# Performance work log

Hardware: AMD Instinct MI355X
Metric: run time of the kernel (lower is better)

Reference implementation:

```python
import jax, jax.numpy as jnp
import numpy as np

N, D_MODEL, NUM_HEAD = 2, 256, 8
HI, WI = 40, 40
MAX_DIS = 7
WS = 2 * MAX_DIS + 1          # 15
HD = D_MODEL // NUM_HEAD      # 32
T = HD ** 0.5
NEG = 1e8                     # fp32 mask value used by the torch module


def setup_inputs() -> dict:
    key = jax.random.key(0)
    ks = jax.random.split(key, 10)
    s = 0.02
    f = lambda i, shape: jax.random.normal(ks[i], shape, jnp.float32)
    return dict(
        q=f(0, (N, D_MODEL, HI, WI)),
        k=f(1, (N, D_MODEL, HI, WI)),
        v=f(2, (N, D_MODEL, HI, WI)),
        Wq=f(3, (D_MODEL, D_MODEL)) * s, bq=jnp.zeros((D_MODEL,), jnp.float32),
        Wk=f(4, (D_MODEL, D_MODEL)) * s, bk=jnp.zeros((D_MODEL,), jnp.float32),
        Wv=f(5, (D_MODEL, D_MODEL)) * s, bv=jnp.zeros((D_MODEL,), jnp.float32),
        rel_k_w=f(6, (NUM_HEAD, WS * WS, HD)) * s,      # grouped 1x1 conv weight
        rel_k_b=jnp.zeros((NUM_HEAD, WS * WS), jnp.float32),
        rel_v=f(7, (NUM_HEAD, HD, WS * WS)) * s,        # nn.Parameter (zeros in torch; random here to exercise math)
        Wp=f(8, (D_MODEL, D_MODEL)) * s, bp=jnp.zeros((D_MODEL,), jnp.float32),
    )


def _geometry(h, w):
    # Static (numpy) index/mask construction matching compute_mask().
    qy = np.repeat(np.arange(h), w)
    qx = np.tile(np.arange(w), h)
    dy = qy[None, :] - qy[:, None]          # key - query, [hw, hw]
    dx = qx[None, :] - qx[:, None]
    valid = (np.abs(dy) <= MAX_DIS) & (np.abs(dx) <= MAX_DIS)
    widx = (np.clip(dy + MAX_DIS, 0, WS - 1) * WS + np.clip(dx + MAX_DIS, 0, WS - 1))
    offs = np.arange(-MAX_DIS, MAX_DIS + 1)
    dyo = np.repeat(offs, WS)               # [ws*ws] row-major window order (dy*WS+dx)
    dxo = np.tile(offs, WS)
    ky = qy[:, None] + dyo[None, :]         # [hw, ws*ws]
    kx = qx[:, None] + dxo[None, :]
    in_img = (ky >= 0) & (ky < h) & (kx >= 0) & (kx < w)
    jidx = np.clip(ky, 0, h - 1) * w + np.clip(kx, 0, w - 1)
    return (jnp.asarray(valid), jnp.asarray(widx), jnp.asarray(in_img), jnp.asarray(jidx))


def reference(q, k, v, Wq, bq, Wk, bk, Wv, bv, rel_k_w, rel_k_b, rel_v, Wp, bp):
    n, c, h, w = q.shape
    hw = h * w
    nh, hd = NUM_HEAD, c // NUM_HEAD

    def proj(x, Wt, b):  # 1x1 conv == per-pixel linear
        return jnp.einsum('oc,ncp->nop', Wt, x.reshape(n, c, hw)) + b[None, :, None]

    qf = proj(q, Wq, bq)
    kf = proj(k, Wk, bk)
    vf = proj(v, Wv, bv)

    qh = qf.reshape(n, nh, hd, hw)
    kh = kf.reshape(n, nh, hd, hw)
    vh = vf.reshape(n, nh, hd, hw)

    # grouped 1x1 conv: per-head linear from hd channels to ws*ws (computed BEFORE q/T)
    rel = jnp.einsum('hwd,nhdp->nhpw', rel_k_w, qh) + rel_k_b[None, :, None, :]  # [n,nh,hw,ws2]

    qh = qh / T
    qk = jnp.einsum('nhdi,nhdj->nhij', qh, kh)   # [n,nh,hw,hw]

    valid, widx, in_img, jidx = _geometry(h, w)

    # --- 'global' path: dense hw x hw, non-local keys masked with -1e8, local keys get rel bias ---
    rel_dense = jnp.take_along_axis(rel, widx[None, None], axis=3)   # [n,nh,hw,hw]
    global_logits = jnp.where(valid[None, None], qk + rel_dense, qk - NEG)
    global_attn = jax.nn.softmax(global_logits, axis=-1)
    agg_value = jnp.einsum('nhij,nhdj->inhd', global_attn, vh).reshape(hw, n, c)

    # --- local path: gather ws*ws window per query; out-of-image keys are -1e8 (pad value), rel added everywhere ---
    gathered = jnp.take_along_axis(qk, jidx[None, None], axis=3)     # [n,nh,hw,ws2]
    local_logits = jnp.where(in_img[None, None], gathered, -NEG) + rel
    local_attn = jax.nn.softmax(local_logits, axis=-1)
    agg_bias = jnp.einsum('nhiw,hdw->inhd', local_attn, rel_v).reshape(hw, n, c)

    out = (agg_value + agg_bias) @ Wp.T + bp    # nn.Linear, output [hw, n, c]
    return out, local_attn
```

## Files before the change

kernel.cpp:

```cpp
#include <hip/hip_runtime.h>
#include <hip/hip_bf16.h>

#define HW    1600
#define NB    2
#define NHEAD 8
#define HD    32
#define WS2   225
#define WDIM  40
#define CDIM  256
#define PROJ  819200
#define RELSTR 248
#define TSC   5.656854249492381f

typedef __attribute__((ext_vector_type(8))) short short8;
typedef __attribute__((ext_vector_type(4))) short short4v;
typedef __attribute__((ext_vector_type(4))) float floatx4;

static __device__ __forceinline__ float bu2f(short u) {
    return __uint_as_float(((unsigned)(unsigned short)u) << 16);
}
static __device__ __forceinline__ short f2bu(float f) {
    __hip_bfloat16 h = __float2bfloat16(f);
    short s; __builtin_memcpy(&s, &h, 2); return s;
}
static __device__ __forceinline__ unsigned pk2(short a, short b) {
    return (unsigned)(unsigned short)a | ((unsigned)(unsigned short)b << 16);
}
static __device__ __forceinline__ float ldf(const void* p, size_t i, bool f32) {
    return f32 ? ((const float*)p)[i] : __bfloat162float(((const __hip_bfloat16*)p)[i]);
}
static __device__ __forceinline__ void st_out(void* p, size_t i, float v, bool f32) {
    if (f32) ((float*)p)[i] = v;
    else     ((__hip_bfloat16*)p)[i] = __float2bfloat16(v);
}

__global__ __launch_bounds__(256) void prep_kernel(
    const void* __restrict__ q, const void* __restrict__ relv,
    const void* __restrict__ Wq, const void* __restrict__ Wk,
    const void* __restrict__ Wv, const void* __restrict__ Wp,
    const void* __restrict__ bq, const void* __restrict__ bk,
    const void* __restrict__ bv, const void* __restrict__ bp,
    const void* __restrict__ rkw, const void* __restrict__ rkb,
    int* __restrict__ flag, __hip_bfloat16* __restrict__ relvT,
    __hip_bfloat16* __restrict__ Wqb, __hip_bfloat16* __restrict__ Wkb,
    __hip_bfloat16* __restrict__ Wvb, __hip_bfloat16* __restrict__ Wpb,
    float* __restrict__ bqf, float* __restrict__ bkf,
    float* __restrict__ bvf, float* __restrict__ bpf,
    __hip_bfloat16* __restrict__ rkwb, __hip_bfloat16* __restrict__ rkbb)
{
    __shared__ int sbad;
    if (threadIdx.x == 0) sbad = 0;
    __syncthreads();
    int bad = 0;
    const __hip_bfloat16* qb = (const __hip_bfloat16*)q;
    for (int i = threadIdx.x; i < 4096; i += 256) {
        float v = __bfloat162float(qb[i]);
        if (!(v > -1e6f && v < 1e6f)) bad = 1;
    }
    if (bad) sbad = 1;
    __syncthreads();
    const bool f32 = (sbad != 0);
    if (blockIdx.x == 0 && threadIdx.x == 0) *flag = sbad;

    const int gid = blockIdx.x * 256 + threadIdx.x;
    const int gsz = gridDim.x * 256;

    for (int e = gid; e < NHEAD * WS2 * HD; e += gsz) {
        const int h = e / (WS2 * HD), idx = e - h * (WS2 * HD);
        const int w = idx >> 5, d = idx & 31;
        relvT[e] = __float2bfloat16(ldf(relv, ((size_t)h * HD + d) * WS2 + w, f32));
    }
    for (int e = gid; e < CDIM * CDIM; e += gsz) {
        Wqb[e] = __float2bfloat16(ldf(Wq, e, f32));
        Wkb[e] = __float2bfloat16(ldf(Wk, e, f32));
        Wvb[e] = __float2bfloat16(ldf(Wv, e, f32));
        Wpb[e] = __float2bfloat16(ldf(Wp, e, f32));
    }
    for (int e = gid; e < CDIM; e += gsz) {
        bqf[e] = ldf(bq, e, f32); bkf[e] = ldf(bk, e, f32);
        bvf[e] = ldf(bv, e, f32); bpf[e] = ldf(bp, e, f32);
    }
    for (int e = gid; e < NHEAD * WS2 * HD; e += gsz)
        rkwb[e] = __float2bfloat16(ldf(rkw, e, f32));
    for (int e = gid; e < NHEAD * WS2; e += gsz)
        rkbb[e] = __float2bfloat16(ldf(rkb, e, f32));
}

__global__ __launch_bounds__(512) void proj_fused(
    const void* __restrict__ xq, const void* __restrict__ xk, const void* __restrict__ xv,
    const __hip_bfloat16* __restrict__ Wqb, const float* __restrict__ bqf,
    const __hip_bfloat16* __restrict__ Wkb, const float* __restrict__ bkf,
    const __hip_bfloat16* __restrict__ Wvb, const float* __restrict__ bvf,
    const int* __restrict__ flag,
    __hip_bfloat16* __restrict__ qs, __hip_bfloat16* __restrict__ ks,
    __hip_bfloat16* __restrict__ vs)
{
    __shared__ short xt[32][264];
    const bool f32 = (*flag != 0);
    const int tid = threadIdx.x;
    const int m0 = blockIdx.x * 32;
    const int n  = blockIdx.y;
    const int t  = blockIdx.z;
    const void* x; const short* W; const float* bias; __hip_bfloat16* dst; float scale;
    if (t == 0)      { x = xq; W = (const short*)Wqb; bias = bqf; dst = qs; scale = 0.17677669529663687f; }
    else if (t == 1) { x = xk; W = (const short*)Wkb; bias = bkf; dst = ks; scale = 1.f; }
    else             { x = xv; W = (const short*)Wvb; bias = bvf; dst = vs; scale = 1.f; }

    {
        const int c  = tid & 255;
        const int gh = tid >> 8;
        const size_t xb = ((size_t)n * CDIM + c) * HW + m0 + gh * 16;
        if (f32) {
            const float* xr = (const float*)x + xb;
            #pragma unroll
            for (int g = 0; g < 4; ++g) {
                float4 f = *(const float4*)(xr + g * 4);
                xt[gh*16 + g*4+0][c] = f2bu(f.x); xt[gh*16 + g*4+1][c] = f2bu(f.y);
                xt[gh*16 + g*4+2][c] = f2bu(f.z); xt[gh*16 + g*4+3][c] = f2bu(f.w);
            }
        } else {
            const __hip_bfloat16* xr = (const __hip_bfloat16*)x + xb;
            short8 s0 = *(const short8*)(xr);
            short8 s1 = *(const short8*)(xr + 8);
            #pragma unroll
            for (int u = 0; u < 8; ++u) {
                xt[gh*16 + u][c]     = s0[u];
                xt[gh*16 + 8 + u][c] = s1[u];
            }
        }
    }
    __syncthreads();

    const int wave = tid >> 6, lane = tid & 63;
    const int m = lane & 15, qd = lane >> 4;

    short8 A[2][8];
    #pragma unroll
    for (int mt = 0; mt < 2; ++mt)
        #pragma unroll
        for (int k = 0; k < 8; ++k)
            A[mt][k] = *(const short8*)(&xt[mt*16 + m][k*32 + qd*8]);

    #pragma unroll
    for (int og = 0; og < 2; ++og) {
        const int o0 = (wave * 2 + og) * 16;
        short8 B[8];
        #pragma unroll
        for (int k = 0; k < 8; ++k)
            B[k] = *(const short8*)(W + (size_t)(o0 + m) * CDIM + k*32 + qd*8);
        floatx4 acc0 = {0,0,0,0}, acc1 = {0,0,0,0};
        #pragma unroll
        for (int k = 0; k < 8; ++k) {
            acc0 = __builtin_amdgcn_mfma_f32_16x16x32_bf16(A[0][k], B[k], acc0, 0, 0, 0);
            acc1 = __builtin_amdgcn_mfma_f32_16x16x32_bf16(A[1][k], B[k], acc1, 0, 0, 0);
        }
        const int o = o0 + (lane & 15), h = o >> 5, d = o & 31;
        const float bv_ = bias[o];
        #pragma unroll
        for (int rg = 0; rg < 4; ++rg) {
            const int p = m0 + (lane >> 4) * 4 + rg;
            dst[((size_t)(n*NHEAD + h)*HW + p)*HD + d]      = __float2bfloat16((acc0[rg] + bv_) * scale);
            dst[((size_t)(n*NHEAD + h)*HW + p + 16)*HD + d] = __float2bfloat16((acc1[rg] + bv_) * scale);
        }
    }
}

#define SP_OFF    0
#define R2_OFF    15616
#define R1_OFF    24064
#define SMAX_OFF  39680
#define SSUM_OFF  39936
#define SMEM_SZ   40192

__global__ __launch_bounds__(256) void attn_mfma(
    const __hip_bfloat16* __restrict__ qs, const __hip_bfloat16* __restrict__ ks,
    const __hip_bfloat16* __restrict__ vs,
    const short* __restrict__ rkwb, const short* __restrict__ rkbb,
    const __hip_bfloat16* __restrict__ relvT,
    const int* __restrict__ flag,
    __hip_bfloat16* __restrict__ agg,
    void* __restrict__ dout)
{
    __shared__ __align__(16) char smem[SMEM_SZ];
    short* sP   = (short*)(smem + SP_OFF);
    short* sRel = (short*)(smem + R2_OFF);
    short* sPw  = (short*)(smem + R2_OFF);
    short* sB   = (short*)(smem + R1_OFF);
    float* sOh  = (float*)(smem + R1_OFF);
    float* sMax = (float*)(smem + SMAX_OFF);
    float* sSum = (float*)(smem + SSUM_OFF);

    const bool f32 = (*flag != 0);
    const int tid = threadIdx.x;
    const int wave = tid >> 6, lane = tid & 63;
    const int m = lane & 15, quad = lane >> 4;
    const int y = blockIdx.x / 3, tile3 = blockIdx.x % 3;
    const int x0 = (tile3 == 0) ? 0 : (tile3 == 1) ? 16 : 24;
    const int wlo = (tile3 == 2) ? 8 : 0;
    const int nh_ = blockIdx.y;
    const int h = nh_ & 7, n = nh_ >> 3;
    const size_t qb = (size_t)nh_ * HW;
    const size_t qrow0 = qb + (size_t)y * WDIM + x0;

    const short8 afrag = *(const short8*)((const short*)qs + (qrow0 + m) * HD + quad * 8);

    for (int wt = wave; wt < 15; wt += 4) {
        const int w0 = wt * 16;
        const int wl = min(w0 + m, WS2 - 1);
        const short8 B = *(const short8*)(rkwb + ((size_t)h * WS2 + wl) * HD + quad * 8);
        floatx4 acc = {0.f, 0.f, 0.f, 0.f};
        acc = __builtin_amdgcn_mfma_f32_16x16x32_bf16(afrag, B, acc, 0, 0, 0);
        const int wcol = w0 + m;
        if (wcol < WS2) {
            const float rb_ = bu2f(rkbb[(size_t)h * WS2 + wcol]);
            #pragma unroll
            for (int rg = 0; rg < 4; ++rg)
                sRel[(quad * 4 + rg) * RELSTR + wcol] = f2bu(acc[rg] * TSC + rb_);
        }
    }
    __syncthreads();

    float L[8][4];
    #pragma unroll
    for (int j = 0; j < 8; ++j)
        #pragma unroll
        for (int rg = 0; rg < 4; ++rg) L[j][rg] = -1e30f;

    #pragma unroll
    for (int j = 0; j < 8; ++j) {
        const int t = wave + 4 * j;
        if (t < 30) {
            const int r = t >> 1, c0_ = (t & 1) << 4;
            const int cc = c0_ + m;
            const int ky = y + r - 7, kxl = x0 - 7 + cc;
            const int gky = min(max(ky, 0), WDIM - 1), gkx = min(max(kxl, 0), WDIM - 1);
            const short8 kfrag = *(const short8*)((const short*)ks + (qb + (size_t)gky * WDIM + gkx) * HD + quad * 8);
            floatx4 s4 = {0.f, 0.f, 0.f, 0.f};
            s4 = __builtin_amdgcn_mfma_f32_16x16x32_bf16(kfrag, afrag, s4, 0, 0, 0);
            const bool kyok = (unsigned)ky < (unsigned)WDIM;
            #pragma unroll
            for (int rg = 0; rg < 4; ++rg) {
                const int kkc = c0_ + quad * 4 + rg;
                const int kx = x0 - 7 + kkc;
                const int dx7 = kkc - m;
                if (kyok && (unsigned)kx < (unsigned)WDIM && (unsigned)dx7 < 15u)
                    L[j][rg] = s4[rg] + bu2f(sRel[m * RELSTR + r * 15 + dx7]);
            }
        }
    }

    float mx = L[0][0];
    #pragma unroll
    for (int j = 0; j < 8; ++j)
        #pragma unroll
        for (int rg = 0; rg < 4; ++rg) mx = fmaxf(mx, L[j][rg]);
    mx = fmaxf(mx, __shfl_xor(mx, 16));
    mx = fmaxf(mx, __shfl_xor(mx, 32));
    if (lane < 16) sMax[lane * 4 + wave] = mx;
    __syncthreads();
    const float4 vM = *(const float4*)&sMax[m * 4];
    const float M = fmaxf(fmaxf(vM.x, vM.y), fmaxf(vM.z, vM.w));
    float sm = 0.f;
    #pragma unroll
    for (int j = 0; j < 8; ++j)
        #pragma unroll
        for (int rg = 0; rg < 4; ++rg) { L[j][rg] = __expf(L[j][rg] - M); sm += L[j][rg]; }
    sm += __shfl_xor(sm, 16);
    sm += __shfl_xor(sm, 32);
    if (lane < 16) sSum[lane * 4 + wave] = sm;
    __syncthreads();
    const float4 vS = *(const float4*)&sSum[m * 4];
    const float inv = 1.f / (vS.x + vS.y + vS.z + vS.w);

    for (int e = tid; e < 16 * 39; e += 256) {
        const int row = e / 39, idx = e - row * 39;
        const int c = (idx < 15) ? idx * 16 + 15 : 240 + (idx - 15);
        sPw[row * 264 + c] = 0;
    }

    #pragma unroll
    for (int j = 0; j < 8; ++j) {
        const int t = wave + 4 * j;
        if (t < 30) {
            const int r = t >> 1, c0_ = (t & 1) << 4;
            const int kb = c0_ + quad * 4;
            short4v pk;
            #pragma unroll
            for (int rg = 0; rg < 4; ++rg) pk[rg] = f2bu(L[j][rg] * inv);
            *(short4v*)(sP + m * 488 + r * 32 + kb) = pk;
            #pragma unroll
            for (int rg = 0; rg < 4; ++rg) {
                const int dx7 = kb + rg - m;
                if ((unsigned)dx7 < 15u) sPw[m * 264 + r * 16 + dx7] = pk[rg];
            }
        }
    }
    __syncthreads();

    #pragma unroll
    for (int rr = 0; rr < 4; ++rr) {
        const int qm = wave * 4 + rr;
        if (qm >= wlo) {
            const size_t obase = (size_t)PROJ + (qrow0 + qm) * WS2;
            #pragma unroll
            for (int c = 0; c < 4; ++c) {
                const int col = lane + 64 * c;
                if (col < WS2) {
                    const int rq = col / 15, dxq = col - rq * 15;
                    st_out(dout, obase + col, bu2f(sPw[qm * 264 + rq * 16 + dxq]), f32);
                }
            }
        }
    }

    for (int half = 0; half < 2; ++half) {
        __syncthreads();
        const int h16 = half << 4;
        {
            unsigned* dstw = (unsigned*)sB;
            for (int p = tid; p < 240; p += 256) {
                const int kk0 = 2 * p;
                const int r = kk0 >> 5, c = kk0 & 31;
                const int gky = min(max(y + r - 7, 0), WDIM - 1);
                const int gkx0 = min(max(x0 - 7 + c, 0), WDIM - 1);
                const int gkx1 = min(max(x0 - 7 + c + 1, 0), WDIM - 1);
                const short* v0 = (const short*)vs + (qb + (size_t)gky * WDIM + gkx0) * HD + h16;
                const short* v1 = (const short*)vs + (qb + (size_t)gky * WDIM + gkx1) * HD + h16;
                const short8 a0 = *(const short8*)v0, b0 = *(const short8*)v1;
                const short8 a1 = *(const short8*)(v0 + 8), b1 = *(const short8*)(v1 + 8);
                #pragma unroll
                for (int dd = 0; dd < 8; ++dd) dstw[dd * 244 + p] = pk2(a0[dd], b0[dd]);
                #pragma unroll
                for (int dd = 0; dd < 8; ++dd) dstw[(dd + 8) * 244 + p] = pk2(a1[dd], b1[dd]);
            }
        }
        __syncthreads();
        floatx4 acc = {0.f, 0.f, 0.f, 0.f};
        for (int u = wave; u < 15; u += 4) {
            const short8 Af = *(const short8*)(sP + m * 488 + u * 32 + quad * 8);
            const short8 Bf = *(const short8*)(sB + m * 488 + u * 32 + quad * 8);
            acc = __builtin_amdgcn_mfma_f32_16x16x32_bf16(Af, Bf, acc, 0, 0, 0);
        }
        __syncthreads();
        {
            unsigned* dstw = (unsigned*)sB;
            for (int p = tid; p < 132; p += 256) {
                short8 a0 = {0,0,0,0,0,0,0,0}, a1 = a0, b0 = a0, b1 = a0;
                if (p < 120) {
                    const int kcol0 = 2 * p;
                    const int r = kcol0 >> 4, dx = kcol0 & 15;
                    const int w0 = r * 15 + dx;
                    const short* rp = (const short*)relvT + ((size_t)h * WS2 + w0) * HD + h16;
                    a0 = *(const short8*)rp; a1 = *(const short8*)(rp + 8);
                    if (dx < 14) {
                        const short* rq = (const short*)relvT + ((size_t)h * WS2 + w0 + 1) * HD + h16;
                        b0 = *(const short8*)rq; b1 = *(const short8*)(rq + 8);
                    }
                }
                #pragma unroll
                for (int dd = 0; dd < 8; ++dd) dstw[dd * 132 + p] = pk2(a0[dd], b0[dd]);
                #pragma unroll
                for (int dd = 0; dd < 8; ++dd) dstw[(dd + 8) * 132 + p] = pk2(a1[dd], b1[dd]);
            }
        }
        __syncthreads();
        for (int u = wave; u < 8; u += 4) {
            const short8 Af = *(const short8*)(sPw + m * 264 + u * 32 + quad * 8);
            const short8 Bf = *(const short8*)(sB + m * 264 + u * 32 + quad * 8);
            acc = __builtin_amdgcn_mfma_f32_16x16x32_bf16(Af, Bf, acc, 0, 0, 0);
        }
        __syncthreads();
        #pragma unroll
        for (int rg = 0; rg < 4; ++rg)
            sOh[wave * 256 + (quad * 4 + rg) * 16 + m] = acc[rg];
        __syncthreads();
        {
            const int qq = tid >> 4, dd = tid & 15;
            const float s = sOh[tid] + sOh[256 + tid] + sOh[512 + tid] + sOh[768 + tid];
            if (qq >= wlo) {
                const size_t i = (size_t)y * WDIM + x0 + qq;
                agg[(i * NB + n) * CDIM + h * HD + h16 + dd] = __float2bfloat16(s);
            }
        }
    }
}

__global__ __launch_bounds__(256) void out_mfma(
    const __hip_bfloat16* __restrict__ agg, const short* __restrict__ Wpb,
    const float* __restrict__ bpf, const int* __restrict__ flag,
    void* __restrict__ dout)
{
    const bool f32 = (*flag != 0);
    const int wave = threadIdx.x >> 6, lane = threadIdx.x & 63;
    const int rb0 = blockIdx.x << 4;
    const int m = lane & 15, qd = lane >> 4;

    const __hip_bfloat16* arow = agg + (size_t)(rb0 + m) * CDIM + qd * 8;
    short8 A[8];
    #pragma unroll
    for (int k = 0; k < 8; ++k)
        A[k] = *(const short8*)(arow + k * 32);

    #pragma unroll
    for (int p = 0; p < 2; ++p) {
        const int o0 = wave * 64 + p * 32;
        floatx4 acc0 = {0.f, 0.f, 0.f, 0.f}, acc1 = {0.f, 0.f, 0.f, 0.f};
        #pragma unroll
        for (int k = 0; k < 8; ++k) {
            short8 b0 = *(const short8*)(Wpb + (size_t)(o0 + m) * CDIM + k * 32 + qd * 8);
            short8 b1 = *(const short8*)(Wpb + (size_t)(o0 + 16 + m) * CDIM + k * 32 + qd * 8);
            acc0 = __builtin_amdgcn_mfma_f32_16x16x32_bf16(A[k], b0, acc0, 0, 0, 0);
            acc1 = __builtin_amdgcn_mfma_f32_16x16x32_bf16(A[k], b1, acc1, 0, 0, 0);
        }
        const int oa = o0 + (lane & 15), ob = oa + 16;
        const float ba_ = bpf[oa];
        const float bb_ = bpf[ob];
        #pragma unroll
        for (int rg = 0; rg < 4; ++rg) {
            const int rb = rb0 + (lane >> 4) * 4 + rg;
            st_out(dout, (size_t)rb * CDIM + oa, acc0[rg] + ba_, f32);
            st_out(dout, (size_t)rb * CDIM + ob, acc1[rg] + bb_, f32);
        }
    }
}

extern "C" void kernel_launch(void* const* d_in, const int* in_sizes, int n_in,
                              void* d_out, int out_size, void* d_ws, size_t ws_size,
                              hipStream_t stream)
{
    const void* q   = d_in[0];
    const void* k   = d_in[1];
    const void* v   = d_in[2];
    const void* Wq  = d_in[3];
    const void* bq  = d_in[4];
    const void* Wk  = d_in[5];
    const void* bk  = d_in[6];
    const void* Wv  = d_in[7];
    const void* bv  = d_in[8];
    const void* rkw = d_in[9];
    const void* rkb = d_in[10];
    const void* rlv = d_in[11];
    const void* Wp  = d_in[12];
    const void* bp  = d_in[13];

    char* wsb = (char*)d_ws;
    int* flag = (int*)wsb;
    __hip_bfloat16* relvT = (__hip_bfloat16*)(wsb + 64);
    __hip_bfloat16* qs    = (__hip_bfloat16*)(wsb + 64 + 115200);
    __hip_bfloat16* ks    = qs + PROJ;
    __hip_bfloat16* vs    = ks + PROJ;
    __hip_bfloat16* agg   = vs + PROJ;
    __hip_bfloat16* Wqb   = (__hip_bfloat16*)(wsb + 6668864);
    __hip_bfloat16* Wkb   = Wqb + CDIM * CDIM;
    __hip_bfloat16* Wvb   = Wkb + CDIM * CDIM;
    __hip_bfloat16* Wpb   = Wvb + CDIM * CDIM;
    __hip_bfloat16* rkwb  = (__hip_bfloat16*)(wsb + 7193152);
    __hip_bfloat16* rkbb  = (__hip_bfloat16*)(wsb + 7308352);
    float* bqf = (float*)(wsb + 7311952);
    float* bkf = bqf + CDIM;
    float* bvf = bkf + CDIM;
    float* bpf = bvf + CDIM;

    prep_kernel<<<128, 256, 0, stream>>>(q, rlv, Wq, Wk, Wv, Wp, bq, bk, bv, bp,
                                         rkw, rkb, flag, relvT,
                                         Wqb, Wkb, Wvb, Wpb, bqf, bkf, bvf, bpf,
                                         rkwb, rkbb);
    proj_fused<<<dim3(50, 2, 3), 512, 0, stream>>>(q, k, v, Wqb, bqf, Wkb, bkf,
                                                   Wvb, bvf, flag, qs, ks, vs);
    attn_mfma<<<dim3(120, 16), 256, 0, stream>>>(qs, ks, vs, (const short*)rkwb,
                                                 (const short*)rkbb, relvT, flag,
                                                 agg, d_out);
    out_mfma<<<200, 256, 0, stream>>>(agg, (const short*)Wpb, bpf, flag, d_out);
}
```

Baseline: 148.3 us.

## Split V staging into two halves to shrink LDS and raise occupancy

Stages the gathered V window into shared memory in two chunks of K rather than one, which halves the staging buffer. The freed space lets the max/sum arrays overlap it, so total LDS drops and launch bounds now ask for five blocks per CU. The cost is extra __syncthreads barriers and a second global-load phase per half, which serialises loading and MFMA work.

```diff
diff --git a/kernel.cpp b/kernel.cpp
--- a/kernel.cpp
+++ b/kernel.cpp
@@ -168,11 +168,11 @@
 #define SP_OFF    0
 #define R2_OFF    15616
 #define R1_OFF    24064
-#define SMAX_OFF  39680
-#define SSUM_OFF  39936
-#define SMEM_SZ   40192
-
-__global__ __launch_bounds__(256) void attn_mfma(
+#define SMAX_OFF  24064
+#define SSUM_OFF  24320
+#define SMEM_SZ   32512
+
+__global__ __launch_bounds__(256, 5) void attn_mfma(
     const __hip_bfloat16* __restrict__ qs, const __hip_bfloat16* __restrict__ ks,
     const __hip_bfloat16* __restrict__ vs,
     const short* __restrict__ rkwb, const short* __restrict__ rkbb,
@@ -317,9 +317,9 @@
         __syncthreads();
         const int h16 = half << 4;
         {
-            unsigned* dstw = (unsigned*)sB;
-            for (int p = tid; p < 240; p += 256) {
-                const int kk0 = 2 * p;
+            if (tid < 128) {
+                unsigned* dstw = (unsigned*)sB;
+                const int kk0 = 2 * tid;
                 const int r = kk0 >> 5, c = kk0 & 31;
                 const int gky = min(max(y + r - 7, 0), WDIM - 1);
                 const int gkx0 = min(max(x0 - 7 + c, 0), WDIM - 1);
@@ -329,16 +329,41 @@
                 const short8 a0 = *(const short8*)v0, b0 = *(const short8*)v1;
                 const short8 a1 = *(const short8*)(v0 + 8), b1 = *(const short8*)(v1 + 8);
                 #pragma unroll
-                for (int dd = 0; dd < 8; ++dd) dstw[dd * 244 + p] = pk2(a0[dd], b0[dd]);
-                #pragma unroll
-                for (int dd = 0; dd < 8; ++dd) dstw[(dd + 8) * 244 + p] = pk2(a1[dd], b1[dd]);
+                for (int dd = 0; dd < 8; ++dd) dstw[dd * 132 + tid] = pk2(a0[dd], b0[dd]);
+                #pragma unroll
+                for (int dd = 0; dd < 8; ++dd) dstw[(dd + 8) * 132 + tid] = pk2(a1[dd], b1[dd]);
             }
         }
         __syncthreads();
         floatx4 acc = {0.f, 0.f, 0.f, 0.f};
-        for (int u = wave; u < 15; u += 4) {
+        for (int u = wave; u < 8; u += 4) {
             const short8 Af = *(const short8*)(sP + m * 488 + u * 32 + quad * 8);
-            const short8 Bf = *(const short8*)(sB + m * 488 + u * 32 + quad * 8);
+            const short8 Bf = *(const short8*)(sB + m * 264 + u * 32 + quad * 8);
+            acc = __builtin_amdgcn_mfma_f32_16x16x32_bf16(Af, Bf, acc, 0, 0, 0);
+        }
+        __syncthreads();
+        {
+            if (tid < 112) {
+                unsigned* dstw = (unsigned*)sB;
+                const int kk0 = 256 + 2 * tid;
+                const int r = kk0 >> 5, c = kk0 & 31;
+                const int gky = min(max(y + r - 7, 0), WDIM - 1);
+                const int gkx0 = min(max(x0 - 7 + c, 0), WDIM - 1);
+                const int gkx1 = min(max(x0 - 7 + c + 1, 0), WDIM - 1);
+                const short* v0 = (const short*)vs + (qb + (size_t)gky * WDIM + gkx0) * HD + h16;
+                const short* v1 = (const short*)vs + (qb + (size_t)gky * WDIM + gkx1) * HD + h16;
+                const short8 a0 = *(const short8*)v0, b0 = *(const short8*)v1;
+                const short8 a1 = *(const short8*)(v0 + 8), b1 = *(const short8*)(v1 + 8);
+                #pragma unroll
+                for (int dd = 0; dd < 8; ++dd) dstw[dd * 132 + tid] = pk2(a0[dd], b0[dd]);
+                #pragma unroll
+                for (int dd = 0; dd < 8; ++dd) dstw[(dd + 8) * 132 + tid] = pk2(a1[dd], b1[dd]);
+            }
+        }
+        __syncthreads();
+        for (int u = 8 + wave; u < 15; u += 4) {
+            const short8 Af = *(const short8*)(sP + m * 488 + u * 32 + quad * 8);
+            const short8 Bf = *(const short8*)(sB + m * 264 + (u - 8) * 32 + quad * 8);
             acc = __builtin_amdgcn_mfma_f32_16x16x32_bf16(Af, Bf, acc, 0, 0, 0);
         }
         __syncthreads();
```

Measured after the change: 147.3 us (median of 2 runs). No clear change (-0.7%).
